# Optimization experiments

Measured on AMD Instinct MI355X. Metric: run time of the kernel, lower is better.

The kernel has to match this reference:

```python
import jax, jax.numpy as jnp
import numpy as np

C = 10.0
EMBEDDING_DIM = 128


def setup_inputs() -> dict:
    key = jax.random.key(0)
    k1, k2 = jax.random.split(key)
    B, P, D, N = 128, 128, 128, 4096
    mh_attn_out = jax.random.normal(k1, (B, P, D), dtype=jnp.float32)
    single_head_key = jax.random.normal(k2, (B, D, N), dtype=jnp.float32)
    mask = jnp.zeros((B, P, N), dtype=jnp.float32)  # additive mask (0 or -inf)
    return {"mh_attn_out": mh_attn_out, "single_head_key": single_head_key, "mask": mask}


def reference(mh_attn_out, single_head_key, mask):
    # score: [B, P, N]
    score = jnp.einsum('bpd,bdn->bpn', mh_attn_out, single_head_key)
    score_scaled = score / jnp.sqrt(jnp.float32(EMBEDDING_DIM))
    score_clipped = C * jnp.tanh(score_scaled)
    score_masked = score_clipped + mask
    probs = jax.nn.softmax(score_masked, axis=-1)
    return probs
```

## Files before the change

### kernel.cpp

```cpp
#include <hip/hip_runtime.h>
#include <math.h>

constexpr int BB = 128;
constexpr int PP = 128;
constexpr int DD = 128;
constexpr int NN = 4096;
constexpr float kC = 10.0f;
constexpr float k2InvSqrtD = 0.1767766952966369f;

constexpr int NTHR = 512;
constexpr int TEL = 272;

typedef float f32x4 __attribute__((ext_vector_type(4)));
typedef _Float16 f16x4 __attribute__((ext_vector_type(4)));
typedef _Float16 f16x8 __attribute__((ext_vector_type(8)));

__device__ __forceinline__ void st_nt_f4(float* p, float4 s) {
    f32x4 v = {s.x, s.y, s.z, s.w};
    __builtin_nontemporal_store(v, (f32x4*)p);
}

__device__ __forceinline__ f16x4 tr_read(unsigned addr) {
    f16x4 r;
    asm volatile("ds_read_b64_tr_b16 %0, %1" : "=v"(r) : "v"(addr));
    return r;
}

__device__ __forceinline__ float clip1(float s, float m) {
    const float e2 = __expf(s * k2InvSqrtD);
    const float r = __builtin_amdgcn_rcpf(e2 + 1.0f);
    return fmaf(-2.0f * kC, r, kC) + m;
}

__global__ __launch_bounds__(NTHR, 3)
void score_kernel(const float* __restrict__ A,
                  const float* __restrict__ K,
                  const float* __restrict__ M,
                  float* __restrict__ O,
                  float* __restrict__ ws) {
    __shared__ _Float16 Khi[32 * TEL];
    __shared__ _Float16 Klo[32 * TEL];

    const int l = blockIdx.x;
    const int b = l >> 5;
    const int ntb = l & 31;
    const int n_base = ntb * 128;

    const int tid = (int)threadIdx.x;
    const int lane = tid & 63;
    const int wid = tid >> 6;
    const int col = lane & 15;
    const int g = lane >> 4;
    const int kbase = 4 * g;

    const float* Arow = A + (size_t)(b * PP + wid * 16 + col) * DD;
    f16x8 ah[4], al[4];
    #pragma unroll
    for (int kb = 0; kb < 4; ++kb) {
        #pragma unroll
        for (int j = 0; j < 8; ++j) {
            const int d = kb * 32 + kbase + (j & 3) + 16 * (j >> 2);
            const float x = Arow[d];
            const _Float16 h = (_Float16)x;
            ah[kb][j] = h;
            al[kb][j] = (_Float16)(x - (float)h);
        }
    }

    const size_t mrow0 = (size_t)(b * PP + wid * 16 + kbase) * NN + n_base + col;
    const unsigned khi0 = (unsigned)(uintptr_t)&Khi[0] + (unsigned)lane * 8u;
    const unsigned klo0 = (unsigned)(uintptr_t)&Klo[0] + (unsigned)lane * 8u;

    const float* Kg = K + (size_t)b * DD * NN + n_base;
    const int nl4 = (tid & 15) * 4;
    const int d0 = tid >> 4;
    const int el0 = ((d0 >> 4) * 4 + (nl4 >> 4)) * TEL + (d0 & 15) * 16 + (nl4 & 12);

    float rsum[4] = {0.f, 0.f, 0.f, 0.f};

    float mv[4], mvn[4];
    #pragma unroll
    for (int j = 0; j < 4; ++j) mv[j] = M[mrow0 + (size_t)j * NN];
    #pragma unroll
    for (int j = 0; j < 4; ++j) mvn[j] = M[mrow0 + (size_t)j * NN + 16];

    #pragma unroll
    for (int half = 0; half < 2; ++half) {
        if (half) __syncthreads();

        #pragma unroll
        for (int i = 0; i < 4; ++i) {
            const float4 v = *(const float4*)(Kg + (size_t)(d0 + 32 * i) * NN
                                              + half * 64 + nl4);
            const float xs[4] = {v.x, v.y, v.z, v.w};
            f16x4 h, lo;
            #pragma unroll
            for (int e = 0; e < 4; ++e) {
                const _Float16 hh = (_Float16)xs[e];
                h[e] = hh;
                lo[e] = (_Float16)(xs[e] - (float)hh);
            }
            const int el = el0 + i * 8 * TEL;
            *(f16x4*)&Khi[el] = h;
            *(f16x4*)&Klo[el] = lo;
        }
        __syncthreads();

        #pragma unroll
        for (int nt2 = 0; nt2 < 4; ++nt2) {
            const int nt = half * 4 + nt2;

            f32x4 acc = {0.f, 0.f, 0.f, 0.f};
            #pragma unroll
            for (int kb = 0; kb < 4; ++kb) {
                const unsigned t0 = (unsigned)(((2 * kb) * 4 + nt2) * 544);
                const f16x4 bh0 = tr_read(khi0 + t0);
                const f16x4 bh1 = tr_read(khi0 + t0 + 4u * 544u);
                const f16x4 bl0 = tr_read(klo0 + t0);
                const f16x4 bl1 = tr_read(klo0 + t0 + 4u * 544u);
                asm volatile("s_waitcnt lgkmcnt(0)" ::: "memory");
                __builtin_amdgcn_sched_barrier(0);
                const f16x8 bh = __builtin_shufflevector(bh0, bh1, 0, 1, 2, 3, 4, 5, 6, 7);
                const f16x8 bl = __builtin_shufflevector(bl0, bl1, 0, 1, 2, 3, 4, 5, 6, 7);
                acc = __builtin_amdgcn_mfma_f32_16x16x32_f16(ah[kb], bh, acc, 0, 0, 0);
                acc = __builtin_amdgcn_mfma_f32_16x16x32_f16(ah[kb], bl, acc, 0, 0, 0);
                acc = __builtin_amdgcn_mfma_f32_16x16x32_f16(al[kb], bh, acc, 0, 0, 0);
            }

            #pragma unroll
            for (int j = 0; j < 4; ++j) {
                const size_t off = mrow0 + (size_t)j * NN + nt * 16;
                const float e = __expf(clip1(acc[j], mv[j]));
                O[off] = e;
                rsum[j] += e;
            }

            #pragma unroll
            for (int j = 0; j < 4; ++j) mv[j] = mvn[j];
            if (nt + 2 < 8) {
                #pragma unroll
                for (int j = 0; j < 4; ++j)
                    mvn[j] = M[mrow0 + (size_t)j * NN + (nt + 2) * 16];
            }
        }
    }

    #pragma unroll
    for (int j = 0; j < 4; ++j) {
        float s = rsum[j];
        s += __shfl_xor(s, 1);
        s += __shfl_xor(s, 2);
        s += __shfl_xor(s, 4);
        s += __shfl_xor(s, 8);
        rsum[j] = s;
    }
    if (col == 0) {
        #pragma unroll
        for (int j = 0; j < 4; ++j)
            ws[(size_t)(b * PP + wid * 16 + kbase + j) * 32 + ntb] = rsum[j];
    }
}

__global__ __launch_bounds__(256, 4)
void scale_kernel(float* __restrict__ O, const float* __restrict__ ws) {
    const int gtid = blockIdx.x * 256 + (int)threadIdx.x;
    const int row = gtid >> 5;
    const int seg = gtid & 31;

    const float* w = ws + (size_t)row * 32;
    float s = 0.f;
    #pragma unroll
    for (int i = 0; i < 8; ++i) {
        const float4 v = *(const float4*)(w + i * 4);
        s += (v.x + v.y) + (v.z + v.w);
    }
    const float inv = __builtin_amdgcn_rcpf(s);

    float4* R = (float4*)(O + (size_t)row * NN);
    #pragma unroll 8
    for (int i = 0; i < 32; ++i) {
        const int idx = i * 32 + seg;
        float4 v = R[idx];
        v.x *= inv; v.y *= inv; v.z *= inv; v.w *= inv;
        st_nt_f4((float*)&R[idx], v);
    }
}

extern "C" void kernel_launch(void* const* d_in, const int* in_sizes, int n_in,
                              void* d_out, int out_size, void* d_ws, size_t ws_size,
                              hipStream_t stream) {
    const float* A = (const float*)d_in[0];
    const float* K = (const float*)d_in[1];
    const float* M = (const float*)d_in[2];
    float* O = (float*)d_out;
    float* ws = (float*)d_ws;

    score_kernel<<<dim3(BB * 32), dim3(NTHR), 0, stream>>>(A, K, M, O, ws);
    scale_kernel<<<dim3(2048), dim3(256), 0, stream>>>(O, ws);
}
```

Before: 273.3 us.

## Halve block size and compute two 16-row tiles per wave to reuse K fragments

Each wave now handles 32 query rows (two 16-row MFMA tiles) instead of 16, so the block shrinks from 512 to 256 threads. Each LDS transposed read of the K fragments now feeds two sets of MFMAs, which halves LDS read traffic per output element. The K staging loop is adjusted so 256 threads still fill the same 128x64 tile. The cost is higher register pressure (twice the A fragments, accumulators, mask values and row sums) and fewer waves per block to hide latency, while launch bounds still ask for 3 blocks per CU.

```diff
diff --git a/kernel.cpp b/kernel.cpp
--- a/kernel.cpp
+++ b/kernel.cpp
@@ -8,7 +8,7 @@
 constexpr float kC = 10.0f;
 constexpr float k2InvSqrtD = 0.1767766952966369f;
 
-constexpr int NTHR = 512;
+constexpr int NTHR = 256;
 constexpr int TEL = 272;
 
 typedef float f32x4 __attribute__((ext_vector_type(4)));
@@ -53,44 +53,51 @@
     const int g = lane >> 4;
     const int kbase = 4 * g;
 
-    const float* Arow = A + (size_t)(b * PP + wid * 16 + col) * DD;
-    f16x8 ah[4], al[4];
-    #pragma unroll
-    for (int kb = 0; kb < 4; ++kb) {
-        #pragma unroll
-        for (int j = 0; j < 8; ++j) {
-            const int d = kb * 32 + kbase + (j & 3) + 16 * (j >> 2);
-            const float x = Arow[d];
-            const _Float16 h = (_Float16)x;
-            ah[kb][j] = h;
-            al[kb][j] = (_Float16)(x - (float)h);
+    f16x8 ah[2][4], al[2][4];
+    #pragma unroll
+    for (int rg = 0; rg < 2; ++rg) {
+        const float* Arow = A + (size_t)(b * PP + wid * 32 + rg * 16 + col) * DD;
+        #pragma unroll
+        for (int kb = 0; kb < 4; ++kb) {
+            #pragma unroll
+            for (int j = 0; j < 8; ++j) {
+                const int d = kb * 32 + kbase + (j & 3) + 16 * (j >> 2);
+                const float x = Arow[d];
+                const _Float16 h = (_Float16)x;
+                ah[rg][kb][j] = h;
+                al[rg][kb][j] = (_Float16)(x - (float)h);
+            }
         }
     }
 
-    const size_t mrow0 = (size_t)(b * PP + wid * 16 + kbase) * NN + n_base + col;
+    const size_t mrow0A = (size_t)(b * PP + wid * 32 + kbase) * NN + n_base + col;
+    const size_t mrow0B = mrow0A + (size_t)16 * NN;
     const unsigned khi0 = (unsigned)(uintptr_t)&Khi[0] + (unsigned)lane * 8u;
     const unsigned klo0 = (unsigned)(uintptr_t)&Klo[0] + (unsigned)lane * 8u;
 
     const float* Kg = K + (size_t)b * DD * NN + n_base;
     const int nl4 = (tid & 15) * 4;
     const int d0 = tid >> 4;
-    const int el0 = ((d0 >> 4) * 4 + (nl4 >> 4)) * TEL + (d0 & 15) * 16 + (nl4 & 12);
-
-    float rsum[4] = {0.f, 0.f, 0.f, 0.f};
-
-    float mv[4], mvn[4];
-    #pragma unroll
-    for (int j = 0; j < 4; ++j) mv[j] = M[mrow0 + (size_t)j * NN];
-    #pragma unroll
-    for (int j = 0; j < 4; ++j) mvn[j] = M[mrow0 + (size_t)j * NN + 16];
+    const int el0 = (nl4 >> 4) * TEL + d0 * 16 + (nl4 & 12);
+
+    float rsum[8] = {0.f, 0.f, 0.f, 0.f, 0.f, 0.f, 0.f, 0.f};
+
+    float mv[8], mvn[8];
+    #pragma unroll
+    for (int j = 0; j < 4; ++j) {
+        mv[j] = M[mrow0A + (size_t)j * NN];
+        mv[4 + j] = M[mrow0B + (size_t)j * NN];
+        mvn[j] = M[mrow0A + (size_t)j * NN + 16];
+        mvn[4 + j] = M[mrow0B + (size_t)j * NN + 16];
+    }
 
     #pragma unroll
     for (int half = 0; half < 2; ++half) {
         if (half) __syncthreads();
 
         #pragma unroll
-        for (int i = 0; i < 4; ++i) {
-            const float4 v = *(const float4*)(Kg + (size_t)(d0 + 32 * i) * NN
+        for (int i = 0; i < 8; ++i) {
+            const float4 v = *(const float4*)(Kg + (size_t)(d0 + 16 * i) * NN
                                               + half * 64 + nl4);
             const float xs[4] = {v.x, v.y, v.z, v.w};
             f16x4 h, lo;
@@ -100,7 +107,7 @@
                 h[e] = hh;
                 lo[e] = (_Float16)(xs[e] - (float)hh);
             }
-            const int el = el0 + i * 8 * TEL;
+            const int el = el0 + i * 4 * TEL;
             *(f16x4*)&Khi[el] = h;
             *(f16x4*)&Klo[el] = lo;
         }
@@ -110,7 +117,8 @@
         for (int nt2 = 0; nt2 < 4; ++nt2) {
             const int nt = half * 4 + nt2;
 
-            f32x4 acc = {0.f, 0.f, 0.f, 0.f};
+            f32x4 accA = {0.f, 0.f, 0.f, 0.f};
+            f32x4 accB = {0.f, 0.f, 0.f, 0.f};
             #pragma unroll
             for (int kb = 0; kb < 4; ++kb) {
                 const unsigned t0 = (unsigned)(((2 * kb) * 4 + nt2) * 544);
@@ -122,42 +130,54 @@
                 __builtin_amdgcn_sched_barrier(0);
                 const f16x8 bh = __builtin_shufflevector(bh0, bh1, 0, 1, 2, 3, 4, 5, 6, 7);
                 const f16x8 bl = __builtin_shufflevector(bl0, bl1, 0, 1, 2, 3, 4, 5, 6, 7);
-                acc = __builtin_amdgcn_mfma_f32_16x16x32_f16(ah[kb], bh, acc, 0, 0, 0);
-                acc = __builtin_amdgcn_mfma_f32_16x16x32_f16(ah[kb], bl, acc, 0, 0, 0);
-                acc = __builtin_amdgcn_mfma_f32_16x16x32_f16(al[kb], bh, acc, 0, 0, 0);
+                accA = __builtin_amdgcn_mfma_f32_16x16x32_f16(ah[0][kb], bh, accA, 0, 0, 0);
+                accA = __builtin_amdgcn_mfma_f32_16x16x32_f16(ah[0][kb], bl, accA, 0, 0, 0);
+                accA = __builtin_amdgcn_mfma_f32_16x16x32_f16(al[0][kb], bh, accA, 0, 0, 0);
+                accB = __builtin_amdgcn_mfma_f32_16x16x32_f16(ah[1][kb], bh, accB, 0, 0, 0);
+                accB = __builtin_amdgcn_mfma_f32_16x16x32_f16(ah[1][kb], bl, accB, 0, 0, 0);
+                accB = __builtin_amdgcn_mfma_f32_16x16x32_f16(al[1][kb], bh, accB, 0, 0, 0);
             }
 
             #pragma unroll
             for (int j = 0; j < 4; ++j) {
-                const size_t off = mrow0 + (size_t)j * NN + nt * 16;
-                const float e = __expf(clip1(acc[j], mv[j]));
-                O[off] = e;
-                rsum[j] += e;
-            }
-
-            #pragma unroll
-            for (int j = 0; j < 4; ++j) mv[j] = mvn[j];
+                const size_t offA = mrow0A + (size_t)j * NN + nt * 16;
+                const float eA = __expf(clip1(accA[j], mv[j]));
+                O[offA] = eA;
+                rsum[j] += eA;
+                const size_t offB = mrow0B + (size_t)j * NN + nt * 16;
+                const float eB = __expf(clip1(accB[j], mv[4 + j]));
+                O[offB] = eB;
+                rsum[4 + j] += eB;
+            }
+
+            #pragma unroll
+            for (int j = 0; j < 8; ++j) mv[j] = mvn[j];
             if (nt + 2 < 8) {
                 #pragma unroll
-                for (int j = 0; j < 4; ++j)
-                    mvn[j] = M[mrow0 + (size_t)j * NN + (nt + 2) * 16];
+                for (int j = 0; j < 4; ++j) {
+                    mvn[j] = M[mrow0A + (size_t)j * NN + (nt + 2) * 16];
+                    mvn[4 + j] = M[mrow0B + (size_t)j * NN + (nt + 2) * 16];
+                }
             }
         }
     }
 
     #pragma unroll
-    for (int j = 0; j < 4; ++j) {
-        float s = rsum[j];
+    for (int q = 0; q < 8; ++q) {
+        float s = rsum[q];
         s += __shfl_xor(s, 1);
         s += __shfl_xor(s, 2);
         s += __shfl_xor(s, 4);
         s += __shfl_xor(s, 8);
-        rsum[j] = s;
+        rsum[q] = s;
     }
     if (col == 0) {
         #pragma unroll
-        for (int j = 0; j < 4; ++j)
-            ws[(size_t)(b * PP + wid * 16 + kbase + j) * 32 + ntb] = rsum[j];
+        for (int rg = 0; rg < 2; ++rg)
+            #pragma unroll
+            for (int j = 0; j < 4; ++j)
+                ws[(size_t)(b * PP + wid * 32 + rg * 16 + kbase + j) * 32 + ntb]
+                    = rsum[rg * 4 + j];
     }
 }
 
```

Measured after the change: 435.0 us. +59.1%, slower.
